# Performance work log

Hardware: AMD Instinct MI355X
Metric: run time of the kernel (lower is better)

Reference implementation:

```python
import jax, jax.numpy as jnp
import numpy as np

V, E, U = 32000, 256, 512  # vocab, embed dim, LSTM units
B, S = 16, 130             # batch, seq len


def lstm_layer(x, mask, k, r, b):
    """Keras LSTMCell semantics. x:[B,T,D], mask:[B,T]; gates order i,f,c,o."""
    h0 = jnp.zeros((x.shape[0], U), x.dtype)
    c0 = h0
    xs = jnp.swapaxes(x, 0, 1)      # [T,B,D]
    ms = jnp.swapaxes(mask, 0, 1)   # [T,B]

    def step(carry, inp):
        h, c = carry
        xt, mt = inp
        z = xt @ k + h @ r + b
        i, f, g, o = jnp.split(z, 4, axis=-1)
        i = jax.nn.sigmoid(i); f = jax.nn.sigmoid(f); o = jax.nn.sigmoid(o)
        cn = f * c + i * jnp.tanh(g)
        hn = o * jnp.tanh(cn)
        m = mt[:, None]
        hn = jnp.where(m, hn, h)  # masked steps carry previous state/output
        cn = jnp.where(m, cn, c)
        return (hn, cn), hn

    _, ys = jax.lax.scan(step, (h0, c0), (xs, ms))
    return jnp.swapaxes(ys, 0, 1)  # [B,T,U]


def stacked_lstm(x, mask, params):
    h = x
    for (k, r, b) in params:
        h = lstm_layer(h, mask, k, r, b)
    return h


def setup_inputs() -> dict:
    key = jax.random.key(0)
    ks = jax.random.split(key, 20)
    d = {}
    d["seqs"] = jax.random.randint(ks[0], (B, S), 0, V)
    d["emb"] = jax.random.normal(ks[1], (V, E), jnp.float32) * 0.01
    i = 2
    for pre in ("f", "b"):
        in_dims = [E, U]
        for l in range(2):
            d[f"{pre}k{l}"] = jax.random.normal(ks[i], (in_dims[l], 4 * U), jnp.float32) * 0.05; i += 1
            d[f"{pre}r{l}"] = jax.random.normal(ks[i], (U, 4 * U), jnp.float32) * 0.05; i += 1
            d[f"{pre}b{l}"] = jnp.zeros((4 * U,), jnp.float32)
    d["Wp"] = jax.random.normal(ks[i], (2 * U, V), jnp.float32) * 0.02
    d["bp"] = jnp.zeros((V,), jnp.float32)
    return d


def reference(seqs, emb, fk0, fr0, fb0, fk1, fr1, fb1, bk0, br0, bb0, bk1, br1, bb1, Wp, bp):
    mask = seqs != 0                 # mask_zero=True
    embedded = emb[seqs]             # [B,S,E]
    # forward LM over tokens 0..S-2
    f = stacked_lstm(embedded[:, :-1], mask[:, :-1], [(fk0, fr0, fb0), (fk1, fr1, fb1)])
    # backward LM over tokens 1..S-1 (go_backwards: scan reversed input)
    xb = embedded[:, 1:][:, ::-1]
    mb = mask[:, 1:][:, ::-1]
    b = stacked_lstm(xb, mb, [(bk0, br0, bb0), (bk1, br1, bb1)])
    b_rev = b[:, ::-1]               # tf.reverse -> chronological order
    o = jnp.concatenate([f[:, :-1], b_rev[:, 1:]], axis=-1)  # [B,S-2,2U]
    return o @ Wp + bp               # [B,S-2,V]
```

## Files before the change

### kernel.cpp

```cpp
#include <hip/hip_runtime.h>

typedef __attribute__((ext_vector_type(8))) short bf16x8;
typedef __attribute__((ext_vector_type(4))) float f32x4;

__device__ __forceinline__ unsigned short f2bf(float x){
  union { float f; unsigned u; } v; v.f = x;
  unsigned r = v.u + 0x7FFFu + ((v.u >> 16) & 1u);
  return (unsigned short)(r >> 16);
}

#define BYPASS_ST_SHORT(base, val) \
  asm volatile("global_store_short %0, %1, off sc0 sc1" :: "v"(base), "v"(val))

__device__ __forceinline__ int ld_flag(const int* p){
  int v;
  asm volatile("global_load_dword %0, %1, off sc0 sc1\n\t"
               "s_waitcnt vmcnt(0)"
               : "=v"(v) : "v"(p) : "memory");
  return v;
}

__device__ __forceinline__ void gload_lds16(const void* g, void* l){
  __builtin_amdgcn_global_load_lds(
      (const __attribute__((address_space(1))) unsigned*)g,
      (__attribute__((address_space(3))) unsigned*)l, 16, 0, 0);
}

__global__ void embed_kernel(const int* __restrict__ seqs, const float* __restrict__ emb,
                             unsigned short* __restrict__ x, int* __restrict__ mask,
                             int* __restrict__ flags){
  const int t = blockIdx.x, b = blockIdx.y, l = threadIdx.x;
  if (t == 0 && b == 0){
    #pragma unroll
    for (int j = 0; j < 16; ++j) flags[l + j*64] = 0;
  }
  const int tok = seqs[b*130 + t];
  if (l == 0) mask[b*130 + t] = (tok != 0) ? 1 : 0;
  const float* src = emb + (size_t)tok * 256;
  unsigned short* dst = x + ((size_t)b*130 + t)*256;
  #pragma unroll
  for (int j = 0; j < 4; ++j) dst[l + j*64] = f2bf(src[l + j*64]);
}

__global__ __launch_bounds__(512) void prep_transpose(
    const float* __restrict__ Wp,  unsigned short* __restrict__ WpT,
    const float* __restrict__ fk0, unsigned short* __restrict__ fk0T,
    const float* __restrict__ fr0, unsigned short* __restrict__ fr0T,
    const float* __restrict__ fk1, unsigned short* __restrict__ fk1T,
    const float* __restrict__ fr1, unsigned short* __restrict__ fr1T,
    const float* __restrict__ bk0, unsigned short* __restrict__ bk0T,
    const float* __restrict__ br0, unsigned short* __restrict__ br0T,
    const float* __restrict__ bk1, unsigned short* __restrict__ bk1T,
    const float* __restrict__ br1, unsigned short* __restrict__ br1T)
{
  __shared__ float tf[32*65];
  const int tid = threadIdx.x;
  const int tx = tid & 63, ty = tid >> 6;
  const int orow = tid & 31, oc = tid >> 5;
  for (int tile = blockIdx.x; tile < 19584; tile += gridDim.x){
    const float* src; unsigned short* dst; int R, C, r0, c0;
    if (tile < 16000){
      src = Wp; dst = WpT; R = 1024; C = 32000;
      const int kt = tile / 500, nt = tile - kt*500;
      r0 = kt*32; c0 = nt*64;
    } else {
      int u = tile - 16000;
      C = 2048;
      if (u < 256)      { src = fk0; dst = fk0T; R = 256;           }
      else if (u < 768) { src = fr0; dst = fr0T; R = 512; u -= 256; }
      else if (u < 1280){ src = fk1; dst = fk1T; R = 512; u -= 768; }
      else if (u < 1792){ src = fr1; dst = fr1T; R = 512; u -= 1280;}
      else if (u < 2048){ src = bk0; dst = bk0T; R = 256; u -= 1792;}
      else if (u < 2560){ src = br0; dst = br0T; R = 512; u -= 2048;}
      else if (u < 3072){ src = bk1; dst = bk1T; R = 512; u -= 2560;}
      else              { src = br1; dst = br1T; R = 512; u -= 3072;}
      const int kt = u >> 5, nt = u & 31;
      r0 = kt*32; c0 = nt*64;
    }
    #pragma unroll
    for (int j = 0; j < 4; ++j)
      tf[(ty + 8*j)*65 + tx] = src[(size_t)(r0 + ty + 8*j)*C + c0 + tx];
    __syncthreads();
    #pragma unroll
    for (int j = 0; j < 4; ++j)
      dst[(size_t)(c0 + oc + 16*j)*R + r0 + orow] = f2bf(tf[orow*65 + oc + 16*j]);
    __syncthreads();
  }
}

__global__ __launch_bounds__(512, 2) void lstm_coop(
    const unsigned short* __restrict__ x, const int* __restrict__ maskg,
    const unsigned short* __restrict__ fk0T, const unsigned short* __restrict__ fr0T,
    const unsigned short* __restrict__ fk1T, const unsigned short* __restrict__ fr1T,
    const unsigned short* __restrict__ bk0T, const unsigned short* __restrict__ br0T,
    const unsigned short* __restrict__ bk1T, const unsigned short* __restrict__ br1T,
    const float* __restrict__ fb0, const float* __restrict__ fb1,
    const float* __restrict__ bb0, const float* __restrict__ bb1,
    unsigned short* h0f, unsigned short* h0b,
    unsigned short* aproj, int* flags)
{
  const int wg = blockIdx.x;
  const int dir = wg >> 5;
  const int layer = (wg >> 4) & 1;
  const int u0 = (wg & 15) * 32;
  const int tid = threadIdx.x;
  const int w = tid >> 6, l = tid & 63;
  const int gate = w >> 1, half = w & 1;
  const int lr = l & 15, lk = l >> 4;
  const int cglob = gate*512 + u0 + half*16 + lr;

  const unsigned short* kT = (layer == 0) ? (dir ? bk0T : fk0T) : (dir ? bk1T : fk1T);
  const unsigned short* rT = (layer == 0) ? (dir ? br0T : fr0T) : (dir ? br1T : fr1T);
  const float* bias = (layer == 0) ? (dir ? bb0 : fb0) : (dir ? bb1 : fb1);
  unsigned short* h0 = dir ? h0b : h0f;

  int* fown  = flags + (layer*2 + dir)*256;
  int* fprod = flags + dir*256;
  int* fself = fown + (wg & 15)*16;

  bf16x8 wreg[16], kreg[16];
  #pragma unroll
  for (int i = 0; i < 16; ++i)
    wreg[i] = *(const bf16x8*)(rT + (size_t)cglob*512 + i*32 + lk*8);
  if (layer == 0){
    #pragma unroll
    for (int i = 0; i < 8; ++i)
      kreg[i] = *(const bf16x8*)(kT + (size_t)cglob*256 + i*32 + lk*8);
  } else {
    #pragma unroll
    for (int i = 0; i < 16; ++i)
      kreg[i] = *(const bf16x8*)(kT + (size_t)cglob*512 + i*32 + lk*8);
  }

  __shared__ float z_lds[4][16][32];
  __shared__ int mask_s[16*130];
  __shared__ __attribute__((aligned(16))) char h_lds[16*1024];
  __shared__ __attribute__((aligned(16))) char h2_lds[16*1024];
  for (int i = tid; i < 16*130; i += 512) mask_s[i] = maskg[i];

  float c_reg = 0.f, h_reg = 0.f;
  const int gu = tid & 31, gb = tid >> 5;
  const float bzi = bias[u0+gu], bzf = bias[512 + u0+gu];
  const float bzc = bias[1024 + u0+gu], bzo = bias[1536 + u0+gu];
  __syncthreads();

  for (int t = 0; t < 128; ++t){
    if (w == 0){
      const int* fp = nullptr; int tgt = 0;
      if (l < 16){ fp = fown + l*16; tgt = t; }
      else if (l < 32 && layer == 1){ fp = fprod + (l-16)*16; tgt = t + 1; }
      if (fp){
        while (ld_flag(fp) < tgt) __builtin_amdgcn_s_sleep(1);
      }
    }
    __syncthreads();

    const int r0s = w*2;
    if (layer == 0){
      if (t > 0){
        #pragma unroll
        for (int j = 0; j < 2; ++j){
          const int r = r0s + j;
          const unsigned short* g = h0 + ((size_t)(t-1)*16 + r)*512 + ((l ^ (r & 7))*8);
          gload_lds16(g, h_lds + r*1024);
        }
      }
    } else {
      #pragma unroll
      for (int j = 0; j < 2; ++j){
        const int r = r0s + j;
        const unsigned short* g = h0 + ((size_t)t*16 + r)*512 + ((l ^ (r & 7))*8);
        gload_lds16(g, h_lds + r*1024);
      }
      if (t > 0){
        const int prow = dir ? (128 - t) : (t - 1);
        #pragma unroll
        for (int j = 0; j < 2; ++j){
          const int r = r0s + j;
          const unsigned short* g = aproj + ((size_t)(r*128 + prow))*1024 + dir*512 + ((l ^ (r & 7))*8);
          gload_lds16(g, h2_lds + r*1024);
        }
      }
    }

    f32x4 acc = {0.f, 0.f, 0.f, 0.f};
    const int fsw = (lr & 7) << 4;
    if (layer == 0){
      const int pos = dir ? (129 - t) : t;
      const unsigned short* xa = x + ((size_t)lr*130 + pos)*256 + lk*8;
      #pragma unroll
      for (int i = 0; i < 8; ++i){
        bf16x8 a = *(const bf16x8*)(xa + i*32);
        acc = __builtin_amdgcn_mfma_f32_16x16x32_bf16(a, kreg[i], acc, 0, 0, 0);
      }
      if (t > 0){
        asm volatile("s_waitcnt vmcnt(0)" ::: "memory");
        __syncthreads();
        #pragma unroll
        for (int i = 0; i < 16; ++i){
          bf16x8 a = *(const bf16x8*)(h_lds + lr*1024 + ((lk*16 + i*64) ^ fsw));
          acc = __builtin_amdgcn_mfma_f32_16x16x32_bf16(a, wreg[i], acc, 0, 0, 0);
        }
      }
    } else {
      asm volatile("s_waitcnt vmcnt(0)" ::: "memory");
      __syncthreads();
      #pragma unroll
      for (int i = 0; i < 16; ++i){
        bf16x8 a = *(const bf16x8*)(h_lds + lr*1024 + ((lk*16 + i*64) ^ fsw));
        acc = __builtin_amdgcn_mfma_f32_16x16x32_bf16(a, kreg[i], acc, 0, 0, 0);
      }
      if (t > 0){
        #pragma unroll
        for (int i = 0; i < 16; ++i){
          bf16x8 a = *(const bf16x8*)(h2_lds + lr*1024 + ((lk*16 + i*64) ^ fsw));
          acc = __builtin_amdgcn_mfma_f32_16x16x32_bf16(a, wreg[i], acc, 0, 0, 0);
        }
      }
    }
    #pragma unroll
    for (int r = 0; r < 4; ++r) z_lds[gate][lk*4 + r][half*16 + lr] = acc[r];
    __syncthreads();

    {
      const float zi = z_lds[0][gb][gu] + bzi;
      const float zf = z_lds[1][gb][gu] + bzf;
      const float zc = z_lds[2][gb][gu] + bzc;
      const float zo = z_lds[3][gb][gu] + bzo;
      const float iv = 1.f / (1.f + expf(-zi));
      const float fv = 1.f / (1.f + expf(-zf));
      const float ov = 1.f / (1.f + expf(-zo));
      const float gv = tanhf(zc);
      float cn = fv*c_reg + iv*gv;
      float hn = ov*tanhf(cn);
      const int pos = dir ? (129 - t) : t;
      if (mask_s[gb*130 + pos] == 0){ cn = c_reg; hn = h_reg; }
      c_reg = cn; h_reg = hn;
      const unsigned short hb = f2bf(hn);
      if (layer == 0){
        unsigned short* p = h0 + ((size_t)t*16 + gb)*512 + u0 + gu;
        BYPASS_ST_SHORT(p, (unsigned)hb);
      } else {
        const int row = dir ? (127 - t) : t;
        unsigned short* p = aproj + ((size_t)gb*128 + row)*1024 + dir*512 + u0 + gu;
        BYPASS_ST_SHORT(p, (unsigned)hb);
      }
    }
    asm volatile("s_waitcnt vmcnt(0)" ::: "memory");
    __syncthreads();
    if (tid == 0){
      int v = t + 1;
      asm volatile("global_store_dword %0, %1, off sc0 sc1" :: "v"(fself), "v"(v) : "memory");
    }
  }
}

__global__ __launch_bounds__(256) void gemm_bf16(
    const unsigned short* __restrict__ A, const unsigned short* __restrict__ Bt,
    const float* __restrict__ bias, float* __restrict__ C,
    int M, int N, int K)
{
  __shared__ unsigned short lA[128*32], lB[128*32];
  const int tid = threadIdx.x;
  const int w = tid >> 6, l = tid & 63;
  const int wr = w >> 1, wc = w & 1;
  const int lr = l & 15, lk = l >> 4;
  const int orig = blockIdx.x;
  const int logical = (orig & 7)*500 + (orig >> 3);
  const int mt = logical & 15;
  const int nt = logical >> 4;
  const int brow = mt * 128, bcol = nt * 128;
  f32x4 acc[4][4] = {};
  for (int k0 = 0; k0 < K; k0 += 32){
    __syncthreads();
    #pragma unroll
    for (int j = 0; j < 2; ++j){
      const int base = w*2048 + j*1024;
      const int L = base + l*16;
      const int Lg = L ^ (((L >> 7) & 3) << 4);
      const int row = Lg >> 6, kb = Lg & 63;
      gload_lds16((const char*)(A + (size_t)(brow+row)*K + k0) + kb, (char*)lA + base);
      gload_lds16((const char*)(Bt + (size_t)(bcol+row)*K + k0) + kb, (char*)lB + base);
    }
    __syncthreads();
    bf16x8 af[4], bfr[4];
    #pragma unroll
    for (int m = 0; m < 4; ++m){
      const int L = (wr*64 + m*16 + lr)*64 + lk*16;
      const int sp = L ^ (((L >> 7) & 3) << 4);
      af[m] = *(const bf16x8*)((char*)lA + sp);
    }
    #pragma unroll
    for (int n = 0; n < 4; ++n){
      const int L = (wc*64 + n*16 + lr)*64 + lk*16;
      const int sp = L ^ (((L >> 7) & 3) << 4);
      bfr[n] = *(const bf16x8*)((char*)lB + sp);
    }
    #pragma unroll
    for (int m = 0; m < 4; ++m)
      #pragma unroll
      for (int n = 0; n < 4; ++n)
        acc[m][n] = __builtin_amdgcn_mfma_f32_16x16x32_bf16(af[m], bfr[n], acc[m][n], 0, 0, 0);
  }
  #pragma unroll
  for (int m = 0; m < 4; ++m){
    #pragma unroll
    for (int n = 0; n < 4; ++n){
      const int col = bcol + wc*64 + n*16 + lr;
      const float bv = bias[col];
      const int row0 = brow + wr*64 + m*16 + lk*4;
      #pragma unroll
      for (int r = 0; r < 4; ++r)
        C[(size_t)(row0 + r)*N + col] = acc[m][n][r] + bv;
    }
  }
}

extern "C" void kernel_launch(void* const* d_in, const int* in_sizes, int n_in,
                              void* d_out, int out_size, void* d_ws, size_t ws_size,
                              hipStream_t stream){
  (void)in_sizes; (void)n_in; (void)out_size; (void)ws_size;
  const int*   seqs = (const int*)d_in[0];
  const float* emb  = (const float*)d_in[1];
  const float* fk0  = (const float*)d_in[2];
  const float* fr0  = (const float*)d_in[3];
  const float* fb0  = (const float*)d_in[4];
  const float* fk1  = (const float*)d_in[5];
  const float* fr1  = (const float*)d_in[6];
  const float* fb1  = (const float*)d_in[7];
  const float* bk0  = (const float*)d_in[8];
  const float* br0  = (const float*)d_in[9];
  const float* bb0  = (const float*)d_in[10];
  const float* bk1  = (const float*)d_in[11];
  const float* br1  = (const float*)d_in[12];
  const float* bb1  = (const float*)d_in[13];
  const float* Wp   = (const float*)d_in[14];
  const float* bp   = (const float*)d_in[15];
  float* out = (float*)d_out;

  char* ws = (char*)d_ws;
  size_t off = 0;
  auto alloc = [&](size_t b){ size_t o = off; off += (b + 255) & ~(size_t)255; return o; };
  int* flags            = (int*)(ws + alloc(4096));
  unsigned short* x     = (unsigned short*)(ws + alloc((size_t)16*130*256*2));
  int* mask             = (int*)(ws + alloc((size_t)16*130*4));
  unsigned short* fk0T  = (unsigned short*)(ws + alloc((size_t)2048*256*2));
  unsigned short* fr0T  = (unsigned short*)(ws + alloc((size_t)2048*512*2));
  unsigned short* fk1T  = (unsigned short*)(ws + alloc((size_t)2048*512*2));
  unsigned short* fr1T  = (unsigned short*)(ws + alloc((size_t)2048*512*2));
  unsigned short* bk0T  = (unsigned short*)(ws + alloc((size_t)2048*256*2));
  unsigned short* br0T  = (unsigned short*)(ws + alloc((size_t)2048*512*2));
  unsigned short* bk1T  = (unsigned short*)(ws + alloc((size_t)2048*512*2));
  unsigned short* br1T  = (unsigned short*)(ws + alloc((size_t)2048*512*2));
  unsigned short* h0f   = (unsigned short*)(ws + alloc((size_t)128*16*512*2));
  unsigned short* h0b   = (unsigned short*)(ws + alloc((size_t)128*16*512*2));
  unsigned short* aproj = (unsigned short*)(ws + alloc((size_t)2048*1024*2));
  unsigned short* WpT   = (unsigned short*)(ws + alloc((size_t)32000*1024*2));

  embed_kernel<<<dim3(130,16), 64, 0, stream>>>(seqs, emb, x, mask, flags);

  prep_transpose<<<256, 512, 0, stream>>>(Wp, WpT,
      fk0, fk0T, fr0, fr0T, fk1, fk1T, fr1, fr1T,
      bk0, bk0T, br0, br0T, bk1, bk1T, br1, br1T);

  lstm_coop<<<64, 512, 0, stream>>>(x, mask,
      fk0T, fr0T, fk1T, fr1T, bk0T, br0T, bk1T, br1T,
      fb0, fb1, bb0, bb1, h0f, h0b, aproj, flags);

  gemm_bf16<<<4000, 256, 0, stream>>>(aproj, WpT, bp, out, 2048, 32000, 1024);
}
```

Before: 871.7 us.

## Double-buffer LDS tiles in output GEMM and widen transpose grid

The projection GEMM now keeps two LDS buffers and issues the global-to-LDS loads for the next K tile before running the MFMAs on the current one, so load latency overlaps compute and one barrier per iteration is dropped. The loop trip count is hardcoded to 32, which assumes K=1024. Separately, the weight transpose/prep kernel is launched with four times as many blocks to raise parallelism. LDS use doubles, which may lower occupancy.

Result: faster. 831.6 us (-4.6%).

```diff
diff --git a/kernel.cpp b/kernel.cpp
--- a/kernel.cpp
+++ b/kernel.cpp
@@ -260,7 +260,7 @@
     const float* __restrict__ bias, float* __restrict__ C,
     int M, int N, int K)
 {
-  __shared__ unsigned short lA[128*32], lB[128*32];
+  __shared__ unsigned short lA[2][128*32], lB[2][128*32];
   const int tid = threadIdx.x;
   const int w = tid >> 6, l = tid & 63;
   const int wr = w >> 1, wc = w & 1;
@@ -270,37 +270,55 @@
   const int mt = logical & 15;
   const int nt = logical >> 4;
   const int brow = mt * 128, bcol = nt * 128;
+
+  const int base0 = w*2048;
+  const int base1 = w*2048 + 1024;
+  const int L0 = base0 + l*16, L1 = base1 + l*16;
+  const int Lg0 = L0 ^ (((L0 >> 7) & 3) << 4);
+  const int Lg1 = L1 ^ (((L1 >> 7) & 3) << 4);
+  const int row0 = Lg0 >> 6, kb0 = Lg0 & 63;
+  const int row1 = Lg1 >> 6, kb1 = Lg1 & 63;
+
   f32x4 acc[4][4] = {};
-  for (int k0 = 0; k0 < K; k0 += 32){
-    __syncthreads();
-    #pragma unroll
-    for (int j = 0; j < 2; ++j){
-      const int base = w*2048 + j*1024;
-      const int L = base + l*16;
-      const int Lg = L ^ (((L >> 7) & 3) << 4);
-      const int row = Lg >> 6, kb = Lg & 63;
-      gload_lds16((const char*)(A + (size_t)(brow+row)*K + k0) + kb, (char*)lA + base);
-      gload_lds16((const char*)(Bt + (size_t)(bcol+row)*K + k0) + kb, (char*)lB + base);
-    }
-    __syncthreads();
+
+  gload_lds16((const char*)(A + (size_t)(brow+row0)*K) + kb0, (char*)lA[0] + base0);
+  gload_lds16((const char*)(Bt + (size_t)(bcol+row0)*K) + kb0, (char*)lB[0] + base0);
+  gload_lds16((const char*)(A + (size_t)(brow+row1)*K) + kb1, (char*)lA[0] + base1);
+  gload_lds16((const char*)(Bt + (size_t)(bcol+row1)*K) + kb1, (char*)lB[0] + base1);
+  asm volatile("s_waitcnt vmcnt(0)" ::: "memory");
+  __syncthreads();
+
+  int cur = 0;
+  for (int kt = 0; kt < 32; ++kt){
+    if (kt < 31){
+      const int k0 = (kt + 1) * 32;
+      const int nb = cur ^ 1;
+      gload_lds16((const char*)(A + (size_t)(brow+row0)*K + k0) + kb0, (char*)lA[nb] + base0);
+      gload_lds16((const char*)(Bt + (size_t)(bcol+row0)*K + k0) + kb0, (char*)lB[nb] + base0);
+      gload_lds16((const char*)(A + (size_t)(brow+row1)*K + k0) + kb1, (char*)lA[nb] + base1);
+      gload_lds16((const char*)(Bt + (size_t)(bcol+row1)*K + k0) + kb1, (char*)lB[nb] + base1);
+    }
     bf16x8 af[4], bfr[4];
     #pragma unroll
     for (int m = 0; m < 4; ++m){
       const int L = (wr*64 + m*16 + lr)*64 + lk*16;
       const int sp = L ^ (((L >> 7) & 3) << 4);
-      af[m] = *(const bf16x8*)((char*)lA + sp);
+      af[m] = *(const bf16x8*)((char*)lA[cur] + sp);
     }
     #pragma unroll
     for (int n = 0; n < 4; ++n){
       const int L = (wc*64 + n*16 + lr)*64 + lk*16;
       const int sp = L ^ (((L >> 7) & 3) << 4);
-      bfr[n] = *(const bf16x8*)((char*)lB + sp);
+      bfr[n] = *(const bf16x8*)((char*)lB[cur] + sp);
     }
     #pragma unroll
     for (int m = 0; m < 4; ++m)
       #pragma unroll
       for (int n = 0; n < 4; ++n)
         acc[m][n] = __builtin_amdgcn_mfma_f32_16x16x32_bf16(af[m], bfr[n], acc[m][n], 0, 0, 0);
+    asm volatile("s_waitcnt vmcnt(0)" ::: "memory");
+    __syncthreads();
+    cur ^= 1;
   }
   #pragma unroll
   for (int m = 0; m < 4; ++m){
@@ -308,10 +326,10 @@
     for (int n = 0; n < 4; ++n){
       const int col = bcol + wc*64 + n*16 + lr;
       const float bv = bias[col];
-      const int row0 = brow + wr*64 + m*16 + lk*4;
+      const int row0_ = brow + wr*64 + m*16 + lk*4;
       #pragma unroll
       for (int r = 0; r < 4; ++r)
-        C[(size_t)(row0 + r)*N + col] = acc[m][n][r] + bv;
+        C[(size_t)(row0_ + r)*N + col] = acc[m][n][r] + bv;
     }
   }
 }
@@ -359,7 +377,7 @@
 
   embed_kernel<<<dim3(130,16), 64, 0, stream>>>(seqs, emb, x, mask, flags);
 
-  prep_transpose<<<256, 512, 0, stream>>>(Wp, WpT,
+  prep_transpose<<<1024, 512, 0, stream>>>(Wp, WpT,
       fk0, fk0T, fr0, fr0T, fk1, fk1T, fr1, fr1T,
       bk0, bk0T, br0, br0T, bk1, bk1T, br1, br1T);
 
```
